# Kernel tuning notes

Hardware: AMD Instinct MI355X
Metric: run time of the kernel (lower is better)

## Reference

```python
import jax, jax.numpy as jnp
import numpy as np

# ---- config (matches init_kwargs) ----
B, NP, DIM, HEADS, DH, NDIM = 32, 576, 512, 8, 64, 16
N = NP + 1                 # seq len incl cls token = 577
INNER = HEADS * DH         # 512


def setup_inputs() -> dict:
    key = jax.random.key(0)
    ks = jax.random.split(key, 11)
    D2 = 2 * DIM  # bidirectional EMA doubles kernel dim
    return {
        "x": jax.random.normal(ks[0], (B, N, DIM), jnp.float32),
        "W_qk": jax.random.normal(ks[1], (DIM, 2 * INNER), jnp.float32) / np.float32(np.sqrt(DIM)),
        "W_v": jax.random.normal(ks[2], (DIM, INNER), jnp.float32) / np.float32(np.sqrt(DIM)),
        "W_out": jax.random.normal(ks[3], (INNER, DIM), jnp.float32) / np.float32(np.sqrt(INNER)),
        "b_out": jnp.zeros((DIM,), jnp.float32),
        "rel_bias": jax.random.normal(ks[4], (2 * N - 1,), jnp.float32) * 0.02,
        "ema_delta": jax.random.normal(ks[5], (D2, NDIM, 1), jnp.float32),
        "ema_alpha": jax.random.normal(ks[6], (D2, NDIM, 1), jnp.float32),
        "ema_beta": jax.random.normal(ks[7], (D2, NDIM, 1), jnp.float32) * 0.5,
        "ema_gamma": jax.random.normal(ks[8], (D2, NDIM), jnp.float32) * 0.5,
        "ema_omega": jax.random.normal(ks[9], (DIM,), jnp.float32),
    }


def _ema_move(x, delta, alpha, beta, gamma, omega):
    """Bidirectional MultiHeadEMA (MEGA) via FFT convolution. x: (B, L, D)."""
    b, L, d = x.shape
    scale = jnp.asarray(np.sqrt(1.0 / NDIM), x.dtype)
    p = jax.nn.sigmoid(delta)                      # (2D, N, 1)
    q = 1.0 - p * jax.nn.sigmoid(alpha)            # (2D, N, 1), in (0,1)
    vander = jnp.arange(L, dtype=x.dtype)[None, None, :] * jnp.log(q)  # (2D, N, L)
    kern = (p * beta) * jnp.exp(vander)            # (2D, N, L)
    k = jnp.einsum('dnl,dn->dl', kern, gamma * scale)  # (2D, L)
    k1, k2 = k[:d], k[d:]
    # combined bidirectional kernel, length 2L-1
    kk = jnp.pad(k1, ((0, 0), (L - 1, 0))) + jnp.pad(k2[:, ::-1], ((0, 0), (0, L - 1)))
    xt = jnp.pad(x.transpose(0, 2, 1), ((0, 0), (0, 0), (L - 1, 0)))  # (B, D, 2L-1)
    fft_len = 2 * L - 1
    nfft = 2 * fft_len
    out = jnp.fft.irfft(jnp.fft.rfft(xt, n=nfft) * jnp.fft.rfft(kk, n=nfft)[None], n=nfft)
    s = 2 * L - 2
    out = out[..., s:s + L].transpose(0, 2, 1).astype(x.dtype)  # (B, L, D)
    return jax.nn.silu(out + x * omega)


def _rel_pos_bias(rb, seq_len):
    """RelativePositionalBias (MEGA): (2*N-1,) param -> (seq_len, seq_len) bias."""
    max_pos = N
    bvec = rb[max_pos - seq_len: max_pos + seq_len - 1]   # (2*seq_len-1,)
    t = jnp.pad(bvec, (0, seq_len))
    t = jnp.tile(t, seq_len)[:-seq_len].reshape(seq_len, 3 * seq_len - 2)
    r = (2 * seq_len - 1) // 2
    return t[:, r:t.shape[1] - r]


def reference(x, W_qk, W_v, W_out, b_out, rel_bias,
              ema_delta, ema_alpha, ema_beta, ema_gamma, ema_omega):
    b, n, _ = x.shape
    cls_tok = x[:, :1]
    moved = _ema_move(x[:, 1:], ema_delta, ema_alpha, ema_beta, ema_gamma, ema_omega)
    xm = jnp.concatenate([cls_tok, moved], axis=1)        # (B, N, DIM)
    q, k = jnp.split(xm @ W_qk, 2, axis=-1)
    v = xm @ W_v                                          # smooth_v_as_well=True

    def heads(t):
        return t.reshape(b, n, HEADS, DH).transpose(0, 2, 1, 3)  # (B, H, N, DH)

    q, k, v = heads(q), heads(k), heads(v)
    dots = jnp.einsum('bhid,bhjd->bhij', q, k) * (DH ** -0.5)
    attn = jax.nn.softmax(dots, axis=-1)
    attn = attn + _rel_pos_bias(rel_bias, n)[None, None]  # bias added AFTER softmax
    out = jnp.einsum('bhij,bhjd->bhid', attn, v)
    out = out.transpose(0, 2, 1, 3).reshape(b, n, INNER)
    return out @ W_out + b_out
```

## Files before the change

### kernel.cpp

```cpp
#include <hip/hip_runtime.h>

typedef unsigned short ushort;

typedef __bf16 bf16x8 __attribute__((ext_vector_type(8)));
typedef float  f32x4  __attribute__((ext_vector_type(4)));
typedef unsigned short u16x8 __attribute__((ext_vector_type(8)));
typedef unsigned short u16x4 __attribute__((ext_vector_type(4)));

static constexpr int BB   = 32;
static constexpr int NN   = 577;
static constexpr int LL   = 576;
static constexpr int DIMC = 512;
static constexpr int BN   = BB * NN;

static constexpr size_t SZ_WQKVT = 1536ull * 512 * 2;
static constexpr size_t SZ_WOUTT = 512ull * 512 * 2;
static constexpr size_t SZ_QK    = (size_t)BN * 1024 * 2;
static constexpr size_t SZ_V     = (size_t)BN * 512 * 2;
static constexpr size_t SZ_VT    = 256ull * 64 * 640 * 2;
static constexpr size_t OFF_WQKVT = 0;
static constexpr size_t OFF_WOUTT = OFF_WQKVT + SZ_WQKVT;
static constexpr size_t OFF_QTAB  = OFF_WOUTT + SZ_WOUTT;
static constexpr size_t OFF_CTAB  = OFF_QTAB + 65536;
static constexpr size_t OFF_QK    = OFF_CTAB + 65536;
static constexpr size_t OFF_V     = OFF_QK + SZ_QK;
static constexpr size_t OFF_REGION= OFF_V + SZ_V;
static constexpr size_t OFF_XM    = OFF_REGION;
static constexpr size_t OFF_VT    = OFF_REGION;
static constexpr size_t OFF_AO    = OFF_REGION + SZ_VT;
static constexpr size_t WS_NEEDED = OFF_AO + SZ_V;

__device__ __forceinline__ ushort bf16bits(float f) {
  unsigned int u = __builtin_bit_cast(unsigned int, f);
  u = (u + 0x7fffu + ((u >> 16) & 1u)) >> 16;
  return (ushort)u;
}
__device__ __forceinline__ float sigmoidf_(float z) { return 1.f / (1.f + __expf(-z)); }
__device__ __forceinline__ float siluf(float z)     { return z / (1.f + __expf(-z)); }
__device__ __forceinline__ float redsum16(float v) {
  v += __shfl_xor(v, 1); v += __shfl_xor(v, 2);
  v += __shfl_xor(v, 4); v += __shfl_xor(v, 8);
  return v;
}

__global__ __launch_bounds__(256) void k_prep(
    const float* __restrict__ delta, const float* __restrict__ alpha,
    const float* __restrict__ beta,  const float* __restrict__ gamma,
    const float* __restrict__ Wqk,   const float* __restrict__ Wv,
    const float* __restrict__ Wout,
    float* __restrict__ qtab, float* __restrict__ ctab,
    ushort* __restrict__ Wqkvt, ushort* __restrict__ Woutt)
{
  int idx = blockIdx.x * 256 + threadIdx.x;
  if (idx < 16384) {
    float p = sigmoidf_(delta[idx]);
    float q = 1.f - p * sigmoidf_(alpha[idx]);
    qtab[idx] = q;
    ctab[idx] = p * beta[idx] * gamma[idx] * 0.25f;
  }
  int i2 = idx - 16384;
  if (i2 >= 0 && i2 < 1536 * 512) {
    int n = i2 >> 9, k = i2 & 511;
    float w = (n < 1024) ? Wqk[k * 1024 + n] : Wv[k * 512 + (n - 1024)];
    Wqkvt[i2] = bf16bits(w);
  }
  int i3 = i2 - 1536 * 512;
  if (i3 >= 0 && i3 < 512 * 512) {
    int n = i3 >> 9, k = i3 & 511;
    Woutt[i3] = bf16bits(Wout[k * 512 + n]);
  }
}

__global__ __launch_bounds__(64) void k_ema_scan(
    const float* __restrict__ x, const float* __restrict__ qtab,
    const float* __restrict__ ctab, float* __restrict__ y1, float* __restrict__ y2)
{
  const int bx = blockIdx.x;
  const int b  = blockIdx.y;
  if (bx < 8) {
    const int d = bx * 64 + threadIdx.x;
    float q[16], c[16], h[16];
    #pragma unroll
    for (int n = 0; n < 16; ++n) { q[n] = qtab[d*16+n]; c[n] = ctab[d*16+n]; h[n] = 0.f; }
    const float* xp = x  + ((size_t)b * NN + 1) * DIMC + d;
    float*       yp = y1 + ((size_t)b * LL)     * DIMC + d;
    float xn[8];
    #pragma unroll
    for (int u = 0; u < 8; ++u) xn[u] = xp[u * DIMC];
    for (int blk = 0; blk < 72; ++blk) {
      float xv[8];
      #pragma unroll
      for (int u = 0; u < 8; ++u) xv[u] = xn[u];
      if (blk < 71) {
        #pragma unroll
        for (int u = 0; u < 8; ++u) xn[u] = xp[((blk + 1) * 8 + u) * DIMC];
      }
      #pragma unroll
      for (int u = 0; u < 8; ++u) {
        float xx = xv[u], y = 0.f;
        #pragma unroll
        for (int n = 0; n < 16; ++n) { h[n] = fmaf(q[n], h[n], xx); y = fmaf(c[n], h[n], y); }
        yp[(blk * 8 + u) * DIMC] = y;
      }
    }
  } else {
    const int d = (bx - 8) * 64 + threadIdx.x;
    float q[16], c[16], g[16];
    #pragma unroll
    for (int n = 0; n < 16; ++n) { q[n] = qtab[(d+512)*16+n]; c[n] = ctab[(d+512)*16+n]; g[n] = 0.f; }
    const float* xp = x  + ((size_t)b * NN + 1) * DIMC + d;
    float*       yp = y2 + ((size_t)b * LL)     * DIMC + d;
    float xn[8];
    #pragma unroll
    for (int u = 0; u < 8; ++u) xn[u] = xp[(568 + u) * DIMC];
    for (int blk = 71; blk >= 0; --blk) {
      float xv[8];
      #pragma unroll
      for (int u = 0; u < 8; ++u) xv[u] = xn[u];
      if (blk > 0) {
        #pragma unroll
        for (int u = 0; u < 8; ++u) xn[u] = xp[((blk - 1) * 8 + u) * DIMC];
      }
      #pragma unroll
      for (int u = 7; u >= 0; --u) {
        float xx = xv[u], y = 0.f;
        #pragma unroll
        for (int n = 0; n < 16; ++n) { g[n] = fmaf(q[n], g[n], xx); y = fmaf(c[n], g[n], y); }
        yp[(blk * 8 + u) * DIMC] = y;
      }
    }
  }
}

__global__ __launch_bounds__(256) void k_ema_comb(
    const float* __restrict__ x, const float* __restrict__ y1,
    const float* __restrict__ y2, const float* __restrict__ omega,
    ushort* __restrict__ xm)
{
  size_t v = (size_t)blockIdx.x * 256 + threadIdx.x;
  size_t e = v * 4;
  int n = (int)(e >> 9);
  int d = (int)(e & 511);
  int b = n / 577;
  int i = n - b * 577;
  f32x4 xv = *(const f32x4*)(x + e);
  u16x4 o;
  if (i == 0) {
    #pragma unroll
    for (int k = 0; k < 4; ++k) o[k] = bf16bits(xv[k]);
  } else {
    size_t ey = ((size_t)b * LL + (i - 1)) * DIMC + d;
    f32x4 a  = *(const f32x4*)(y1 + ey);
    f32x4 c2 = *(const f32x4*)(y2 + ey);
    f32x4 om = *(const f32x4*)(omega + d);
    #pragma unroll
    for (int k = 0; k < 4; ++k) o[k] = bf16bits(siluf(a[k] + c2[k] + xv[k] * om[k]));
  }
  *(u16x4*)(xm + e) = o;
}

__global__ __launch_bounds__(256) void k_qkv(
    const ushort* __restrict__ A, const ushort* __restrict__ Bt,
    ushort* __restrict__ qk, ushort* __restrict__ v)
{
  __shared__ alignas(16) ushort lA[128 * 40];
  __shared__ alignas(16) ushort lB[128 * 40];
  const int tid = threadIdx.x, wv = tid >> 6, lane = tid & 63;
  const int quad = lane >> 4, c16 = lane & 15;
  const int row0 = blockIdx.y * 128, n0 = blockIdx.x * 128;
  const int wm = (wv >> 1) * 64, wn = (wv & 1) * 64;
  f32x4 z4 = {0.f, 0.f, 0.f, 0.f};
  f32x4 acc[4][4];
  #pragma unroll
  for (int mi = 0; mi < 4; ++mi)
    #pragma unroll
    for (int ni = 0; ni < 4; ++ni) acc[mi][ni] = z4;

  for (int kt = 0; kt < 16; ++kt) {
    const int k0 = kt * 32;
    u16x8 sa[2], sb[2];
    #pragma unroll
    for (int it = 0; it < 2; ++it) {
      int ch = it * 256 + tid;
      int r = ch >> 2, cc = ch & 3;
      int grow = row0 + r; if (grow > BN - 1) grow = BN - 1;
      sa[it] = *(const u16x8*)(A + (size_t)grow * 512 + k0 + cc * 8);
      sb[it] = *(const u16x8*)(Bt + (size_t)(n0 + r) * 512 + k0 + cc * 8);
    }
    __syncthreads();
    #pragma unroll
    for (int it = 0; it < 2; ++it) {
      int ch = it * 256 + tid;
      int r = ch >> 2, cc = ch & 3;
      *(u16x8*)(lA + r * 40 + cc * 8) = sa[it];
      *(u16x8*)(lB + r * 40 + cc * 8) = sb[it];
    }
    __syncthreads();
    bf16x8 af[4], bfv[4];
    #pragma unroll
    for (int mi = 0; mi < 4; ++mi)
      af[mi] = *(const bf16x8*)(lA + (wm + mi * 16 + c16) * 40 + quad * 8);
    #pragma unroll
    for (int ni = 0; ni < 4; ++ni)
      bfv[ni] = *(const bf16x8*)(lB + (wn + ni * 16 + c16) * 40 + quad * 8);
    #pragma unroll
    for (int mi = 0; mi < 4; ++mi)
      #pragma unroll
      for (int ni = 0; ni < 4; ++ni)
        acc[mi][ni] = __builtin_amdgcn_mfma_f32_16x16x32_bf16(af[mi], bfv[ni], acc[mi][ni], 0, 0, 0);
  }
  const bool isv = (n0 >= 1024);
  const float osc = (n0 < 512) ? 0.125f : 1.0f;
  #pragma unroll
  for (int mi = 0; mi < 4; ++mi) {
    #pragma unroll
    for (int r = 0; r < 4; ++r) {
      int grow = row0 + wm + mi * 16 + quad * 4 + r;
      if (grow < BN) {
        #pragma unroll
        for (int ni = 0; ni < 4; ++ni) {
          int col = n0 + wn + ni * 16 + c16;
          ushort vb = bf16bits(acc[mi][ni][r] * osc);
          if (!isv) qk[(size_t)grow * 1024 + col] = vb;
          else      v[(size_t)grow * 512 + (col - 1024)] = vb;
        }
      }
    }
  }
}

__global__ __launch_bounds__(256) void k_vtrans(
    const ushort* __restrict__ v, ushort* __restrict__ vt)
{
  __shared__ alignas(16) ushort lt[64 * 72];
  const int tid = threadIdx.x;
  const int bh = blockIdx.y, b = bh >> 3, h = bh & 7;
  const int j0 = blockIdx.x * 64;
  #pragma unroll
  for (int pass = 0; pass < 2; ++pass) {
    int cch = pass * 256 + tid;
    int jl = cch >> 3, cc = cch & 7;
    int gj = j0 + jl;
    u16x8 val = {0, 0, 0, 0, 0, 0, 0, 0};
    if (gj < 577) val = *(const u16x8*)(v + ((size_t)(b * NN + gj)) * 512 + h * 64 + cc * 8);
    *(u16x8*)(lt + jl * 72 + cc * 8) = val;
  }
  __syncthreads();
  #pragma unroll
  for (int pass = 0; pass < 2; ++pass) {
    int cch = pass * 256 + tid;
    int dh = cch >> 3, jc = cch & 7;
    u16x8 o;
    #pragma unroll
    for (int e = 0; e < 8; ++e) o[e] = lt[(jc * 8 + e) * 72 + dh];
    *(u16x8*)(vt + ((size_t)(bh * 64 + dh)) * 640 + j0 + jc * 8) = o;
  }
}

__global__ __launch_bounds__(256) void k_fattn(
    const ushort* __restrict__ qk, const ushort* __restrict__ vt,
    const float* __restrict__ relb, ushort* __restrict__ ao)
{
  __shared__ alignas(16) ushort lq[128 * 64];
  __shared__ alignas(16) ushort lk[64 * 64];
  __shared__ alignas(16) ushort lv[64 * 64];
  __shared__ alignas(16) ushort lp[128 * 64];
  __shared__ ushort lbias16[1280];
  const int tid = threadIdx.x, wv = tid >> 6, lane = tid & 63;
  const int quad = lane >> 4, c16 = lane & 15;
  const int hc16 = c16 >> 3, lo16 = c16 & 7;
  const int bh = blockIdx.y, b = bh >> 3, h = bh & 7;
  const int i0 = blockIdx.x * 128, wm = wv * 32;
  for (int t = tid; t < 1280; t += 256) {
    int idx = t - 64;
    lbias16[t] = (idx >= 0 && idx < 1153) ? bf16bits(relb[idx]) : (ushort)0;
  }
  #pragma unroll
  for (int it = 0; it < 4; ++it) {
    int ch = it * 256 + tid;
    int r = ch >> 3, cc = ch & 7;
    int gi = i0 + r; if (gi > 576) gi = 576;
    *(u16x8*)(lq + r * 64 + ((cc ^ (r & 7)) * 8)) =
        *(const u16x8*)(qk + ((size_t)(b * NN + gi)) * 1024 + h * 64 + cc * 8);
  }
  float lsum[2][4];
  #pragma unroll
  for (int ms = 0; ms < 2; ++ms)
    #pragma unroll
    for (int r = 0; r < 4; ++r) lsum[ms][r] = 0.f;
  f32x4 z4 = {0.f, 0.f, 0.f, 0.f};
  f32x4 accp[2][4], accb[2][4];
  #pragma unroll
  for (int ms = 0; ms < 2; ++ms)
    #pragma unroll
    for (int ns = 0; ns < 4; ++ns) { accp[ms][ns] = z4; accb[ms][ns] = z4; }

  for (int jt = 0; jt < 10; ++jt) {
    const int j0 = jt * 64;
    u16x8 sk[2], sv[2];
    #pragma unroll
    for (int it = 0; it < 2; ++it) {
      int ch = it * 256 + tid;
      int r = ch >> 3, cc = ch & 7;
      int gj = j0 + r; if (gj > 576) gj = 576;
      sk[it] = *(const u16x8*)(qk + ((size_t)(b * NN + gj)) * 1024 + 512 + h * 64 + cc * 8);
      sv[it] = *(const u16x8*)(vt + ((size_t)(bh * 64 + r)) * 640 + j0 + cc * 8);
    }
    __syncthreads();
    #pragma unroll
    for (int it = 0; it < 2; ++it) {
      int ch = it * 256 + tid;
      int r = ch >> 3, cc = ch & 7;
      int pc = (cc ^ (r & 7)) * 8;
      *(u16x8*)(lk + r * 64 + pc) = sk[it];
      *(u16x8*)(lv + r * 64 + pc) = sv[it];
    }
    __syncthreads();
    f32x4 dacc[2][4];
    #pragma unroll
    for (int ms = 0; ms < 2; ++ms)
      #pragma unroll
      for (int ns = 0; ns < 4; ++ns) dacc[ms][ns] = z4;
    #pragma unroll
    for (int kk = 0; kk < 2; ++kk) {
      bf16x8 aq[2], bk[4];
      const int ck = kk * 4 + quad;
      #pragma unroll
      for (int ms = 0; ms < 2; ++ms) {
        const int row = wm + ms * 16 + c16;
        aq[ms] = *(const bf16x8*)(lq + row * 64 + ((ck ^ (row & 7)) * 8));
      }
      #pragma unroll
      for (int ns = 0; ns < 4; ++ns) {
        const int row = ns * 16 + c16;
        bk[ns] = *(const bf16x8*)(lk + row * 64 + ((ck ^ (row & 7)) * 8));
      }
      #pragma unroll
      for (int ms = 0; ms < 2; ++ms)
        #pragma unroll
        for (int ns = 0; ns < 4; ++ns)
          dacc[ms][ns] = __builtin_amdgcn_mfma_f32_16x16x32_bf16(aq[ms], bk[ns], dacc[ms][ns], 0, 0, 0);
    }
    #pragma unroll
    for (int ms = 0; ms < 2; ++ms) {
      #pragma unroll
      for (int r = 0; r < 4; ++r) {
        float ex[4];
        #pragma unroll
        for (int ns = 0; ns < 4; ++ns) {
          float e = __expf(dacc[ms][ns][r]);
          if (jt == 9 && (j0 + ns * 16 + c16) >= 577) e = 0.f;
          ex[ns] = e;
        }
        lsum[ms][r] += (ex[0] + ex[1]) + (ex[2] + ex[3]);
        const int lrow = wm + ms * 16 + quad * 4 + r;
        const int xr = lrow & 7;
        #pragma unroll
        for (int ns = 0; ns < 4; ++ns)
          lp[lrow * 64 + (((ns * 2 + hc16) ^ xr) * 8) + lo16] = bf16bits(ex[ns]);
      }
    }
    __syncthreads();
    #pragma unroll
    for (int kk = 0; kk < 2; ++kk) {
      bf16x8 ap[2], ab[2], bV[4];
      const int ck = kk * 4 + quad;
      #pragma unroll
      for (int ms = 0; ms < 2; ++ms) {
        const int row = wm + ms * 16 + c16;
        ap[ms] = *(const bf16x8*)(lp + row * 64 + ((ck ^ (row & 7)) * 8));
      }
      #pragma unroll
      for (int ms = 0; ms < 2; ++ms) {
        u16x8 abu;
        const int base = 64 + 576 + j0 + kk * 32 + quad * 8 - (i0 + wm + ms * 16 + c16);
        #pragma unroll
        for (int e = 0; e < 8; ++e) abu[e] = lbias16[base + e];
        ab[ms] = __builtin_bit_cast(bf16x8, abu);
      }
      #pragma unroll
      for (int ns = 0; ns < 4; ++ns) {
        const int row = ns * 16 + c16;
        bV[ns] = *(const bf16x8*)(lv + row * 64 + ((ck ^ (row & 7)) * 8));
      }
      #pragma unroll
      for (int ms = 0; ms < 2; ++ms)
        #pragma unroll
        for (int ns = 0; ns < 4; ++ns) {
          accp[ms][ns] = __builtin_amdgcn_mfma_f32_16x16x32_bf16(ap[ms], bV[ns], accp[ms][ns], 0, 0, 0);
          accb[ms][ns] = __builtin_amdgcn_mfma_f32_16x16x32_bf16(ab[ms], bV[ns], accb[ms][ns], 0, 0, 0);
        }
    }
  }
  float li[2][4];
  #pragma unroll
  for (int ms = 0; ms < 2; ++ms)
    #pragma unroll
    for (int r = 0; r < 4; ++r) li[ms][r] = 1.f / redsum16(lsum[ms][r]);
  #pragma unroll
  for (int ms = 0; ms < 2; ++ms)
    #pragma unroll
    for (int r = 0; r < 4; ++r) {
      int ii = i0 + wm + ms * 16 + quad * 4 + r;
      if (ii < 577) {
        #pragma unroll
        for (int ns = 0; ns < 4; ++ns)
          ao[((size_t)(b * NN + ii)) * 512 + h * 64 + ns * 16 + c16] =
              bf16bits(accp[ms][ns][r] * li[ms][r] + accb[ms][ns][r]);
      }
    }
}

__global__ __launch_bounds__(256) void k_out(
    const ushort* __restrict__ A, const ushort* __restrict__ Bt,
    const float* __restrict__ bout, float* __restrict__ out)
{
  __shared__ alignas(16) ushort lA[128 * 40];
  __shared__ alignas(16) ushort lB[128 * 40];
  const int tid = threadIdx.x, wv = tid >> 6, lane = tid & 63;
  const int quad = lane >> 4, c16 = lane & 15;
  const int row0 = blockIdx.y * 128, n0 = blockIdx.x * 128;
  const int wm = (wv >> 1) * 64, wn = (wv & 1) * 64;
  f32x4 z4 = {0.f, 0.f, 0.f, 0.f};
  f32x4 acc[4][4];
  #pragma unroll
  for (int mi = 0; mi < 4; ++mi)
    #pragma unroll
    for (int ni = 0; ni < 4; ++ni) acc[mi][ni] = z4;

  for (int kt = 0; kt < 16; ++kt) {
    const int k0 = kt * 32;
    u16x8 sa[2], sb[2];
    #pragma unroll
    for (int it = 0; it < 2; ++it) {
      int ch = it * 256 + tid;
      int r = ch >> 2, cc = ch & 3;
      int grow = row0 + r; if (grow > BN - 1) grow = BN - 1;
      sa[it] = *(const u16x8*)(A + (size_t)grow * 512 + k0 + cc * 8);
      sb[it] = *(const u16x8*)(Bt + (size_t)(n0 + r) * 512 + k0 + cc * 8);
    }
    __syncthreads();
    #pragma unroll
    for (int it = 0; it < 2; ++it) {
      int ch = it * 256 + tid;
      int r = ch >> 2, cc = ch & 3;
      *(u16x8*)(lA + r * 40 + cc * 8) = sa[it];
      *(u16x8*)(lB + r * 40 + cc * 8) = sb[it];
    }
    __syncthreads();
    bf16x8 af[4], bfv[4];
    #pragma unroll
    for (int mi = 0; mi < 4; ++mi)
      af[mi] = *(const bf16x8*)(lA + (wm + mi * 16 + c16) * 40 + quad * 8);
    #pragma unroll
    for (int ni = 0; ni < 4; ++ni)
      bfv[ni] = *(const bf16x8*)(lB + (wn + ni * 16 + c16) * 40 + quad * 8);
    #pragma unroll
    for (int mi = 0; mi < 4; ++mi)
      #pragma unroll
      for (int ni = 0; ni < 4; ++ni)
        acc[mi][ni] = __builtin_amdgcn_mfma_f32_16x16x32_bf16(af[mi], bfv[ni], acc[mi][ni], 0, 0, 0);
  }
  #pragma unroll
  for (int mi = 0; mi < 4; ++mi) {
    #pragma unroll
    for (int r = 0; r < 4; ++r) {
      int grow = row0 + wm + mi * 16 + quad * 4 + r;
      if (grow < BN) {
        #pragma unroll
        for (int ni = 0; ni < 4; ++ni) {
          int col = n0 + wn + ni * 16 + c16;
          out[(size_t)grow * 512 + col] = acc[mi][ni][r] + bout[col];
        }
      }
    }
  }
}

extern "C" void kernel_launch(void* const* d_in, const int* in_sizes, int n_in,
                              void* d_out, int out_size, void* d_ws, size_t ws_size,
                              hipStream_t stream) {
  (void)in_sizes; (void)n_in; (void)out_size;
  if (ws_size < WS_NEEDED) return;
  const float* x    = (const float*)d_in[0];
  const float* Wqk  = (const float*)d_in[1];
  const float* Wv   = (const float*)d_in[2];
  const float* Wout = (const float*)d_in[3];
  const float* bout = (const float*)d_in[4];
  const float* relb = (const float*)d_in[5];
  const float* edel = (const float*)d_in[6];
  const float* ealp = (const float*)d_in[7];
  const float* ebet = (const float*)d_in[8];
  const float* egam = (const float*)d_in[9];
  const float* eome = (const float*)d_in[10];

  char* ws = (char*)d_ws;
  ushort* Wqkvt = (ushort*)(ws + OFF_WQKVT);
  ushort* Woutt = (ushort*)(ws + OFF_WOUTT);
  float*  qtab  = (float*)(ws + OFF_QTAB);
  float*  ctab  = (float*)(ws + OFF_CTAB);
  ushort* qkb   = (ushort*)(ws + OFF_QK);
  ushort* vb    = (ushort*)(ws + OFF_V);
  ushort* xm    = (ushort*)(ws + OFF_XM);
  ushort* vtb   = (ushort*)(ws + OFF_VT);
  ushort* aob   = (ushort*)(ws + OFF_AO);
  float*  outp  = (float*)d_out;
  float*  y1    = outp;
  float*  y2    = (float*)(ws + OFF_QK);

  k_prep<<<dim3(4160), dim3(256), 0, stream>>>(edel, ealp, ebet, egam, Wqk, Wv, Wout,
                                               qtab, ctab, Wqkvt, Woutt);
  k_ema_scan<<<dim3(16, 32), dim3(64), 0, stream>>>(x, qtab, ctab, y1, y2);
  k_ema_comb<<<dim3(9232), dim3(256), 0, stream>>>(x, y1, y2, eome, xm);
  k_qkv<<<dim3(12, 145), dim3(256), 0, stream>>>(xm, Wqkvt, qkb, vb);
  k_vtrans<<<dim3(10, 256), dim3(256), 0, stream>>>(vb, vtb);
  k_fattn<<<dim3(5, 256), dim3(256), 0, stream>>>(qkb, vtb, relb, aob);
  k_out<<<dim3(4, 145), dim3(256), 0, stream>>>(aob, Woutt, bout, outp);
}
```

Baseline: 364.8 us.

## Prefetch next K-tiles in GEMMs and split rel-bias@V into separate kernel

```diff
diff --git a/kernel.cpp b/kernel.cpp
--- a/kernel.cpp
+++ b/kernel.cpp
@@ -35,6 +35,10 @@
   u = (u + 0x7fffu + ((u >> 16) & 1u)) >> 16;
   return (ushort)u;
 }
+__device__ __forceinline__ float bf2f(ushort u) {
+  unsigned int x = ((unsigned int)u) << 16;
+  return __builtin_bit_cast(float, x);
+}
 __device__ __forceinline__ float sigmoidf_(float z) { return 1.f / (1.f + __expf(-z)); }
 __device__ __forceinline__ float siluf(float z)     { return z / (1.f + __expf(-z)); }
 __device__ __forceinline__ float redsum16(float v) {
@@ -176,17 +180,16 @@
     #pragma unroll
     for (int ni = 0; ni < 4; ++ni) acc[mi][ni] = z4;
 
+  u16x8 sa[2], sb[2];
+  #pragma unroll
+  for (int it = 0; it < 2; ++it) {
+    int ch = it * 256 + tid;
+    int r = ch >> 2, cc = ch & 3;
+    int grow = row0 + r; if (grow > BN - 1) grow = BN - 1;
+    sa[it] = *(const u16x8*)(A + (size_t)grow * 512 + cc * 8);
+    sb[it] = *(const u16x8*)(Bt + (size_t)(n0 + r) * 512 + cc * 8);
+  }
   for (int kt = 0; kt < 16; ++kt) {
-    const int k0 = kt * 32;
-    u16x8 sa[2], sb[2];
-    #pragma unroll
-    for (int it = 0; it < 2; ++it) {
-      int ch = it * 256 + tid;
-      int r = ch >> 2, cc = ch & 3;
-      int grow = row0 + r; if (grow > BN - 1) grow = BN - 1;
-      sa[it] = *(const u16x8*)(A + (size_t)grow * 512 + k0 + cc * 8);
-      sb[it] = *(const u16x8*)(Bt + (size_t)(n0 + r) * 512 + k0 + cc * 8);
-    }
     __syncthreads();
     #pragma unroll
     for (int it = 0; it < 2; ++it) {
@@ -196,6 +199,17 @@
       *(u16x8*)(lB + r * 40 + cc * 8) = sb[it];
     }
     __syncthreads();
+    if (kt < 15) {
+      const int k0 = (kt + 1) * 32;
+      #pragma unroll
+      for (int it = 0; it < 2; ++it) {
+        int ch = it * 256 + tid;
+        int r = ch >> 2, cc = ch & 3;
+        int grow = row0 + r; if (grow > BN - 1) grow = BN - 1;
+        sa[it] = *(const u16x8*)(A + (size_t)grow * 512 + k0 + cc * 8);
+        sb[it] = *(const u16x8*)(Bt + (size_t)(n0 + r) * 512 + k0 + cc * 8);
+      }
+    }
     bf16x8 af[4], bfv[4];
     #pragma unroll
     for (int mi = 0; mi < 4; ++mi)
@@ -257,55 +271,134 @@
   }
 }
 
-__global__ __launch_bounds__(256) void k_fattn(
+__global__ __launch_bounds__(256, 4) void k_biasv(
+    const ushort* __restrict__ vt, const float* __restrict__ relb,
+    ushort* __restrict__ ao)
+{
+  __shared__ alignas(16) ushort lv[64 * 64];
+  __shared__ ushort lbias16[1280];
+  const int tid = threadIdx.x, wv = tid >> 6, lane = tid & 63;
+  const int quad = lane >> 4, c16 = lane & 15;
+  const int bh = blockIdx.y, b = bh >> 3, h = bh & 7;
+  const int i0 = blockIdx.x * 128, wm = wv * 32;
+  for (int t = tid; t < 1280; t += 256) {
+    int idx = t - 64;
+    lbias16[t] = (idx >= 0 && idx < 1153) ? bf16bits(relb[idx]) : (ushort)0;
+  }
+  f32x4 z4 = {0.f, 0.f, 0.f, 0.f};
+  f32x4 acc[2][4];
+  #pragma unroll
+  for (int ms = 0; ms < 2; ++ms)
+    #pragma unroll
+    for (int ns = 0; ns < 4; ++ns) acc[ms][ns] = z4;
+
+  u16x8 sv[2];
+  #pragma unroll
+  for (int it = 0; it < 2; ++it) {
+    int ch = it * 256 + tid;
+    int r = ch >> 3, cc = ch & 7;
+    sv[it] = *(const u16x8*)(vt + ((size_t)(bh * 64 + r)) * 640 + cc * 8);
+  }
+  for (int jt = 0; jt < 10; ++jt) {
+    const int j0 = jt * 64;
+    __syncthreads();
+    #pragma unroll
+    for (int it = 0; it < 2; ++it) {
+      int ch = it * 256 + tid;
+      int r = ch >> 3, cc = ch & 7;
+      *(u16x8*)(lv + r * 64 + ((cc ^ (r & 7)) * 8)) = sv[it];
+    }
+    __syncthreads();
+    if (jt < 9) {
+      #pragma unroll
+      for (int it = 0; it < 2; ++it) {
+        int ch = it * 256 + tid;
+        int r = ch >> 3, cc = ch & 7;
+        sv[it] = *(const u16x8*)(vt + ((size_t)(bh * 64 + r)) * 640 + j0 + 64 + cc * 8);
+      }
+    }
+    #pragma unroll
+    for (int kk = 0; kk < 2; ++kk) {
+      bf16x8 ab[2], bV[4];
+      const int ck = kk * 4 + quad;
+      #pragma unroll
+      for (int ms = 0; ms < 2; ++ms) {
+        u16x8 abu;
+        const int base = 64 + 576 + j0 + kk * 32 + quad * 8 - (i0 + wm + ms * 16 + c16);
+        #pragma unroll
+        for (int e = 0; e < 8; ++e) abu[e] = lbias16[base + e];
+        ab[ms] = __builtin_bit_cast(bf16x8, abu);
+      }
+      #pragma unroll
+      for (int ns = 0; ns < 4; ++ns) {
+        const int row = ns * 16 + c16;
+        bV[ns] = *(const bf16x8*)(lv + row * 64 + ((ck ^ (row & 7)) * 8));
+      }
+      #pragma unroll
+      for (int ms = 0; ms < 2; ++ms)
+        #pragma unroll
+        for (int ns = 0; ns < 4; ++ns)
+          acc[ms][ns] = __builtin_amdgcn_mfma_f32_16x16x32_bf16(ab[ms], bV[ns], acc[ms][ns], 0, 0, 0);
+    }
+  }
+  #pragma unroll
+  for (int ms = 0; ms < 2; ++ms)
+    #pragma unroll
+    for (int r = 0; r < 4; ++r) {
+      int ii = i0 + wm + ms * 16 + quad * 4 + r;
+      if (ii < 577) {
+        #pragma unroll
+        for (int ns = 0; ns < 4; ++ns)
+          ao[((size_t)(b * NN + ii)) * 512 + h * 64 + ns * 16 + c16] =
+              bf16bits(acc[ms][ns][r]);
+      }
+    }
+}
+
+__global__ __launch_bounds__(256, 4) void k_fattn(
     const ushort* __restrict__ qk, const ushort* __restrict__ vt,
-    const float* __restrict__ relb, ushort* __restrict__ ao)
-{
-  __shared__ alignas(16) ushort lq[128 * 64];
+    ushort* __restrict__ ao)
+{
   __shared__ alignas(16) ushort lk[64 * 64];
   __shared__ alignas(16) ushort lv[64 * 64];
   __shared__ alignas(16) ushort lp[128 * 64];
-  __shared__ ushort lbias16[1280];
   const int tid = threadIdx.x, wv = tid >> 6, lane = tid & 63;
   const int quad = lane >> 4, c16 = lane & 15;
   const int hc16 = c16 >> 3, lo16 = c16 & 7;
   const int bh = blockIdx.y, b = bh >> 3, h = bh & 7;
   const int i0 = blockIdx.x * 128, wm = wv * 32;
-  for (int t = tid; t < 1280; t += 256) {
-    int idx = t - 64;
-    lbias16[t] = (idx >= 0 && idx < 1153) ? bf16bits(relb[idx]) : (ushort)0;
-  }
-  #pragma unroll
-  for (int it = 0; it < 4; ++it) {
+  bf16x8 aq[2][2];
+  #pragma unroll
+  for (int ms = 0; ms < 2; ++ms) {
+    int gi = i0 + wm + ms * 16 + c16; if (gi > 576) gi = 576;
+    const ushort* qrow = qk + ((size_t)(b * NN + gi)) * 1024 + h * 64;
+    #pragma unroll
+    for (int kk = 0; kk < 2; ++kk)
+      aq[ms][kk] = *(const bf16x8*)(qrow + kk * 32 + quad * 8);
+  }
+  float lsum[2][4];
+  #pragma unroll
+  for (int ms = 0; ms < 2; ++ms)
+    #pragma unroll
+    for (int r = 0; r < 4; ++r) lsum[ms][r] = 0.f;
+  f32x4 z4 = {0.f, 0.f, 0.f, 0.f};
+  f32x4 accp[2][4];
+  #pragma unroll
+  for (int ms = 0; ms < 2; ++ms)
+    #pragma unroll
+    for (int ns = 0; ns < 4; ++ns) accp[ms][ns] = z4;
+
+  u16x8 sk[2], sv[2];
+  #pragma unroll
+  for (int it = 0; it < 2; ++it) {
     int ch = it * 256 + tid;
     int r = ch >> 3, cc = ch & 7;
-    int gi = i0 + r; if (gi > 576) gi = 576;
-    *(u16x8*)(lq + r * 64 + ((cc ^ (r & 7)) * 8)) =
-        *(const u16x8*)(qk + ((size_t)(b * NN + gi)) * 1024 + h * 64 + cc * 8);
-  }
-  float lsum[2][4];
-  #pragma unroll
-  for (int ms = 0; ms < 2; ++ms)
-    #pragma unroll
-    for (int r = 0; r < 4; ++r) lsum[ms][r] = 0.f;
-  f32x4 z4 = {0.f, 0.f, 0.f, 0.f};
-  f32x4 accp[2][4], accb[2][4];
-  #pragma unroll
-  for (int ms = 0; ms < 2; ++ms)
-    #pragma unroll
-    for (int ns = 0; ns < 4; ++ns) { accp[ms][ns] = z4; accb[ms][ns] = z4; }
-
+    int gj = r; if (gj > 576) gj = 576;
+    sk[it] = *(const u16x8*)(qk + ((size_t)(b * NN + gj)) * 1024 + 512 + h * 64 + cc * 8);
+    sv[it] = *(const u16x8*)(vt + ((size_t)(bh * 64 + r)) * 640 + cc * 8);
+  }
   for (int jt = 0; jt < 10; ++jt) {
     const int j0 = jt * 64;
-    u16x8 sk[2], sv[2];
-    #pragma unroll
-    for (int it = 0; it < 2; ++it) {
-      int ch = it * 256 + tid;
-      int r = ch >> 3, cc = ch & 7;
-      int gj = j0 + r; if (gj > 576) gj = 576;
-      sk[it] = *(const u16x8*)(qk + ((size_t)(b * NN + gj)) * 1024 + 512 + h * 64 + cc * 8);
-      sv[it] = *(const u16x8*)(vt + ((size_t)(bh * 64 + r)) * 640 + j0 + cc * 8);
-    }
     __syncthreads();
     #pragma unroll
     for (int it = 0; it < 2; ++it) {
@@ -316,6 +409,17 @@
       *(u16x8*)(lv + r * 64 + pc) = sv[it];
     }
     __syncthreads();
+    if (jt < 9) {
+      const int jn = j0 + 64;
+      #pragma unroll
+      for (int it = 0; it < 2; ++it) {
+        int ch = it * 256 + tid;
+        int r = ch >> 3, cc = ch & 7;
+        int gj = jn + r; if (gj > 576) gj = 576;
+        sk[it] = *(const u16x8*)(qk + ((size_t)(b * NN + gj)) * 1024 + 512 + h * 64 + cc * 8);
+        sv[it] = *(const u16x8*)(vt + ((size_t)(bh * 64 + r)) * 640 + jn + cc * 8);
+      }
+    }
     f32x4 dacc[2][4];
     #pragma unroll
     for (int ms = 0; ms < 2; ++ms)
@@ -323,13 +427,8 @@
       for (int ns = 0; ns < 4; ++ns) dacc[ms][ns] = z4;
     #pragma unroll
     for (int kk = 0; kk < 2; ++kk) {
-      bf16x8 aq[2], bk[4];
+      bf16x8 bk[4];
       const int ck = kk * 4 + quad;
-      #pragma unroll
-      for (int ms = 0; ms < 2; ++ms) {
-        const int row = wm + ms * 16 + c16;
-        aq[ms] = *(const bf16x8*)(lq + row * 64 + ((ck ^ (row & 7)) * 8));
-      }
       #pragma unroll
       for (int ns = 0; ns < 4; ++ns) {
         const int row = ns * 16 + c16;
@@ -339,7 +438,7 @@
       for (int ms = 0; ms < 2; ++ms)
         #pragma unroll
         for (int ns = 0; ns < 4; ++ns)
-          dacc[ms][ns] = __builtin_amdgcn_mfma_f32_16x16x32_bf16(aq[ms], bk[ns], dacc[ms][ns], 0, 0, 0);
+          dacc[ms][ns] = __builtin_amdgcn_mfma_f32_16x16x32_bf16(aq[ms][kk], bk[ns], dacc[ms][ns], 0, 0, 0);
     }
     #pragma unroll
     for (int ms = 0; ms < 2; ++ms) {
@@ -363,7 +462,7 @@
     __syncthreads();
     #pragma unroll
     for (int kk = 0; kk < 2; ++kk) {
-      bf16x8 ap[2], ab[2], bV[4];
+      bf16x8 ap[2], bV[4];
       const int ck = kk * 4 + quad;
       #pragma unroll
       for (int ms = 0; ms < 2; ++ms) {
@@ -371,14 +470,6 @@
         ap[ms] = *(const bf16x8*)(lp + row * 64 + ((ck ^ (row & 7)) * 8));
       }
       #pragma unroll
-      for (int ms = 0; ms < 2; ++ms) {
-        u16x8 abu;
-        const int base = 64 + 576 + j0 + kk * 32 + quad * 8 - (i0 + wm + ms * 16 + c16);
-        #pragma unroll
-        for (int e = 0; e < 8; ++e) abu[e] = lbias16[base + e];
-        ab[ms] = __builtin_bit_cast(bf16x8, abu);
-      }
-      #pragma unroll
       for (int ns = 0; ns < 4; ++ns) {
         const int row = ns * 16 + c16;
         bV[ns] = *(const bf16x8*)(lv + row * 64 + ((ck ^ (row & 7)) * 8));
@@ -386,10 +477,8 @@
       #pragma unroll
       for (int ms = 0; ms < 2; ++ms)
         #pragma unroll
-        for (int ns = 0; ns < 4; ++ns) {
+        for (int ns = 0; ns < 4; ++ns)
           accp[ms][ns] = __builtin_amdgcn_mfma_f32_16x16x32_bf16(ap[ms], bV[ns], accp[ms][ns], 0, 0, 0);
-          accb[ms][ns] = __builtin_amdgcn_mfma_f32_16x16x32_bf16(ab[ms], bV[ns], accb[ms][ns], 0, 0, 0);
-        }
     }
   }
   float li[2][4];
@@ -404,9 +493,11 @@
       int ii = i0 + wm + ms * 16 + quad * 4 + r;
       if (ii < 577) {
         #pragma unroll
-        for (int ns = 0; ns < 4; ++ns)
-          ao[((size_t)(b * NN + ii)) * 512 + h * 64 + ns * 16 + c16] =
-              bf16bits(accp[ms][ns][r] * li[ms][r] + accb[ms][ns][r]);
+        for (int ns = 0; ns < 4; ++ns) {
+          size_t idx = ((size_t)(b * NN + ii)) * 512 + h * 64 + ns * 16 + c16;
+          float ob = bf2f(ao[idx]);
+          ao[idx] = bf16bits(fmaf(accp[ms][ns][r], li[ms][r], ob));
+        }
       }
     }
 }
@@ -428,17 +519,16 @@
     #pragma unroll
     for (int ni = 0; ni < 4; ++ni) acc[mi][ni] = z4;
 
+  u16x8 sa[2], sb[2];
+  #pragma unroll
+  for (int it = 0; it < 2; ++it) {
+    int ch = it * 256 + tid;
+    int r = ch >> 2, cc = ch & 3;
+    int grow = row0 + r; if (grow > BN - 1) grow = BN - 1;
+    sa[it] = *(const u16x8*)(A + (size_t)grow * 512 + cc * 8);
+    sb[it] = *(const u16x8*)(Bt + (size_t)(n0 + r) * 512 + cc * 8);
+  }
   for (int kt = 0; kt < 16; ++kt) {
-    const int k0 = kt * 32;
-    u16x8 sa[2], sb[2];
-    #pragma unroll
-    for (int it = 0; it < 2; ++it) {
-      int ch = it * 256 + tid;
-      int r = ch >> 2, cc = ch & 3;
-      int grow = row0 + r; if (grow > BN - 1) grow = BN - 1;
-      sa[it] = *(const u16x8*)(A + (size_t)grow * 512 + k0 + cc * 8);
-      sb[it] = *(const u16x8*)(Bt + (size_t)(n0 + r) * 512 + k0 + cc * 8);
-    }
     __syncthreads();
     #pragma unroll
     for (int it = 0; it < 2; ++it) {
@@ -448,6 +538,17 @@
       *(u16x8*)(lB + r * 40 + cc * 8) = sb[it];
     }
     __syncthreads();
+    if (kt < 15) {
+      const int k0 = (kt + 1) * 32;
+      #pragma unroll
+      for (int it = 0; it < 2; ++it) {
+        int ch = it * 256 + tid;
+        int r = ch >> 2, cc = ch & 3;
+        int grow = row0 + r; if (grow > BN - 1) grow = BN - 1;
+        sa[it] = *(const u16x8*)(A + (size_t)grow * 512 + k0 + cc * 8);
+        sb[it] = *(const u16x8*)(Bt + (size_t)(n0 + r) * 512 + k0 + cc * 8);
+      }
+    }
     bf16x8 af[4], bfv[4];
     #pragma unroll
     for (int mi = 0; mi < 4; ++mi)
@@ -514,6 +615,7 @@
   k_ema_comb<<<dim3(9232), dim3(256), 0, stream>>>(x, y1, y2, eome, xm);
   k_qkv<<<dim3(12, 145), dim3(256), 0, stream>>>(xm, Wqkvt, qkb, vb);
   k_vtrans<<<dim3(10, 256), dim3(256), 0, stream>>>(vb, vtb);
-  k_fattn<<<dim3(5, 256), dim3(256), 0, stream>>>(qkb, vtb, relb, aob);
+  k_biasv<<<dim3(5, 256), dim3(256), 0, stream>>>(vtb, relb, aob);
+  k_fattn<<<dim3(5, 256), dim3(256), 0, stream>>>(qkb, vtb, aob);
   k_out<<<dim3(4, 145), dim3(256), 0, stream>>>(aob, Woutt, bout, outp);
 }
```

Result: slower. 548.0 us (+50.2%).

## Prefetch next tile into registers in GEMM and attention kernels; keep Q in registers

Applied to the files above, without the earlier changes.

```diff
diff --git a/kernel.cpp b/kernel.cpp
--- a/kernel.cpp
+++ b/kernel.cpp
@@ -176,17 +176,16 @@
     #pragma unroll
     for (int ni = 0; ni < 4; ++ni) acc[mi][ni] = z4;
 
+  u16x8 sa[2], sb[2];
+  #pragma unroll
+  for (int it = 0; it < 2; ++it) {
+    int ch = it * 256 + tid;
+    int r = ch >> 2, cc = ch & 3;
+    int grow = row0 + r; if (grow > BN - 1) grow = BN - 1;
+    sa[it] = *(const u16x8*)(A + (size_t)grow * 512 + cc * 8);
+    sb[it] = *(const u16x8*)(Bt + (size_t)(n0 + r) * 512 + cc * 8);
+  }
   for (int kt = 0; kt < 16; ++kt) {
-    const int k0 = kt * 32;
-    u16x8 sa[2], sb[2];
-    #pragma unroll
-    for (int it = 0; it < 2; ++it) {
-      int ch = it * 256 + tid;
-      int r = ch >> 2, cc = ch & 3;
-      int grow = row0 + r; if (grow > BN - 1) grow = BN - 1;
-      sa[it] = *(const u16x8*)(A + (size_t)grow * 512 + k0 + cc * 8);
-      sb[it] = *(const u16x8*)(Bt + (size_t)(n0 + r) * 512 + k0 + cc * 8);
-    }
     __syncthreads();
     #pragma unroll
     for (int it = 0; it < 2; ++it) {
@@ -196,6 +195,17 @@
       *(u16x8*)(lB + r * 40 + cc * 8) = sb[it];
     }
     __syncthreads();
+    if (kt < 15) {
+      const int k0 = (kt + 1) * 32;
+      #pragma unroll
+      for (int it = 0; it < 2; ++it) {
+        int ch = it * 256 + tid;
+        int r = ch >> 2, cc = ch & 3;
+        int grow = row0 + r; if (grow > BN - 1) grow = BN - 1;
+        sa[it] = *(const u16x8*)(A + (size_t)grow * 512 + k0 + cc * 8);
+        sb[it] = *(const u16x8*)(Bt + (size_t)(n0 + r) * 512 + k0 + cc * 8);
+      }
+    }
     bf16x8 af[4], bfv[4];
     #pragma unroll
     for (int mi = 0; mi < 4; ++mi)
@@ -261,7 +271,6 @@
     const ushort* __restrict__ qk, const ushort* __restrict__ vt,
     const float* __restrict__ relb, ushort* __restrict__ ao)
 {
-  __shared__ alignas(16) ushort lq[128 * 64];
   __shared__ alignas(16) ushort lk[64 * 64];
   __shared__ alignas(16) ushort lv[64 * 64];
   __shared__ alignas(16) ushort lp[128 * 64];
@@ -275,13 +284,14 @@
     int idx = t - 64;
     lbias16[t] = (idx >= 0 && idx < 1153) ? bf16bits(relb[idx]) : (ushort)0;
   }
-  #pragma unroll
-  for (int it = 0; it < 4; ++it) {
-    int ch = it * 256 + tid;
-    int r = ch >> 3, cc = ch & 7;
-    int gi = i0 + r; if (gi > 576) gi = 576;
-    *(u16x8*)(lq + r * 64 + ((cc ^ (r & 7)) * 8)) =
-        *(const u16x8*)(qk + ((size_t)(b * NN + gi)) * 1024 + h * 64 + cc * 8);
+  bf16x8 aq[2][2];
+  #pragma unroll
+  for (int ms = 0; ms < 2; ++ms) {
+    int gi = i0 + wm + ms * 16 + c16; if (gi > 576) gi = 576;
+    const ushort* qrow = qk + ((size_t)(b * NN + gi)) * 1024 + h * 64;
+    #pragma unroll
+    for (int kk = 0; kk < 2; ++kk)
+      aq[ms][kk] = *(const bf16x8*)(qrow + kk * 32 + quad * 8);
   }
   float lsum[2][4];
   #pragma unroll
@@ -295,17 +305,17 @@
     #pragma unroll
     for (int ns = 0; ns < 4; ++ns) { accp[ms][ns] = z4; accb[ms][ns] = z4; }
 
+  u16x8 sk[2], sv[2];
+  #pragma unroll
+  for (int it = 0; it < 2; ++it) {
+    int ch = it * 256 + tid;
+    int r = ch >> 3, cc = ch & 7;
+    int gj = r; if (gj > 576) gj = 576;
+    sk[it] = *(const u16x8*)(qk + ((size_t)(b * NN + gj)) * 1024 + 512 + h * 64 + cc * 8);
+    sv[it] = *(const u16x8*)(vt + ((size_t)(bh * 64 + r)) * 640 + cc * 8);
+  }
   for (int jt = 0; jt < 10; ++jt) {
     const int j0 = jt * 64;
-    u16x8 sk[2], sv[2];
-    #pragma unroll
-    for (int it = 0; it < 2; ++it) {
-      int ch = it * 256 + tid;
-      int r = ch >> 3, cc = ch & 7;
-      int gj = j0 + r; if (gj > 576) gj = 576;
-      sk[it] = *(const u16x8*)(qk + ((size_t)(b * NN + gj)) * 1024 + 512 + h * 64 + cc * 8);
-      sv[it] = *(const u16x8*)(vt + ((size_t)(bh * 64 + r)) * 640 + j0 + cc * 8);
-    }
     __syncthreads();
     #pragma unroll
     for (int it = 0; it < 2; ++it) {
@@ -316,6 +326,17 @@
       *(u16x8*)(lv + r * 64 + pc) = sv[it];
     }
     __syncthreads();
+    if (jt < 9) {
+      const int jn = j0 + 64;
+      #pragma unroll
+      for (int it = 0; it < 2; ++it) {
+        int ch = it * 256 + tid;
+        int r = ch >> 3, cc = ch & 7;
+        int gj = jn + r; if (gj > 576) gj = 576;
+        sk[it] = *(const u16x8*)(qk + ((size_t)(b * NN + gj)) * 1024 + 512 + h * 64 + cc * 8);
+        sv[it] = *(const u16x8*)(vt + ((size_t)(bh * 64 + r)) * 640 + jn + cc * 8);
+      }
+    }
     f32x4 dacc[2][4];
     #pragma unroll
     for (int ms = 0; ms < 2; ++ms)
@@ -323,13 +344,8 @@
       for (int ns = 0; ns < 4; ++ns) dacc[ms][ns] = z4;
     #pragma unroll
     for (int kk = 0; kk < 2; ++kk) {
-      bf16x8 aq[2], bk[4];
+      bf16x8 bk[4];
       const int ck = kk * 4 + quad;
-      #pragma unroll
-      for (int ms = 0; ms < 2; ++ms) {
-        const int row = wm + ms * 16 + c16;
-        aq[ms] = *(const bf16x8*)(lq + row * 64 + ((ck ^ (row & 7)) * 8));
-      }
       #pragma unroll
       for (int ns = 0; ns < 4; ++ns) {
         const int row = ns * 16 + c16;
@@ -339,7 +355,7 @@
       for (int ms = 0; ms < 2; ++ms)
         #pragma unroll
         for (int ns = 0; ns < 4; ++ns)
-          dacc[ms][ns] = __builtin_amdgcn_mfma_f32_16x16x32_bf16(aq[ms], bk[ns], dacc[ms][ns], 0, 0, 0);
+          dacc[ms][ns] = __builtin_amdgcn_mfma_f32_16x16x32_bf16(aq[ms][kk], bk[ns], dacc[ms][ns], 0, 0, 0);
     }
     #pragma unroll
     for (int ms = 0; ms < 2; ++ms) {
@@ -406,7 +422,7 @@
         #pragma unroll
         for (int ns = 0; ns < 4; ++ns)
           ao[((size_t)(b * NN + ii)) * 512 + h * 64 + ns * 16 + c16] =
-              bf16bits(accp[ms][ns][r] * li[ms][r] + accb[ms][ns][r]);
+              bf16bits(fmaf(accp[ms][ns][r], li[ms][r], accb[ms][ns][r]));
       }
     }
 }
@@ -428,17 +444,16 @@
     #pragma unroll
     for (int ni = 0; ni < 4; ++ni) acc[mi][ni] = z4;
 
+  u16x8 sa[2], sb[2];
+  #pragma unroll
+  for (int it = 0; it < 2; ++it) {
+    int ch = it * 256 + tid;
+    int r = ch >> 2, cc = ch & 3;
+    int grow = row0 + r; if (grow > BN - 1) grow = BN - 1;
+    sa[it] = *(const u16x8*)(A + (size_t)grow * 512 + cc * 8);
+    sb[it] = *(const u16x8*)(Bt + (size_t)(n0 + r) * 512 + cc * 8);
+  }
   for (int kt = 0; kt < 16; ++kt) {
-    const int k0 = kt * 32;
-    u16x8 sa[2], sb[2];
-    #pragma unroll
-    for (int it = 0; it < 2; ++it) {
-      int ch = it * 256 + tid;
-      int r = ch >> 2, cc = ch & 3;
-      int grow = row0 + r; if (grow > BN - 1) grow = BN - 1;
-      sa[it] = *(const u16x8*)(A + (size_t)grow * 512 + k0 + cc * 8);
-      sb[it] = *(const u16x8*)(Bt + (size_t)(n0 + r) * 512 + k0 + cc * 8);
-    }
     __syncthreads();
     #pragma unroll
     for (int it = 0; it < 2; ++it) {
@@ -448,6 +463,17 @@
       *(u16x8*)(lB + r * 40 + cc * 8) = sb[it];
     }
     __syncthreads();
+    if (kt < 15) {
+      const int k0 = (kt + 1) * 32;
+      #pragma unroll
+      for (int it = 0; it < 2; ++it) {
+        int ch = it * 256 + tid;
+        int r = ch >> 2, cc = ch & 3;
+        int grow = row0 + r; if (grow > BN - 1) grow = BN - 1;
+        sa[it] = *(const u16x8*)(A + (size_t)grow * 512 + k0 + cc * 8);
+        sb[it] = *(const u16x8*)(Bt + (size_t)(n0 + r) * 512 + k0 + cc * 8);
+      }
+    }
     bf16x8 af[4], bfv[4];
     #pragma unroll
     for (int mi = 0; mi < 4; ++mi)
```

Measured after the change: 367.5 us. About the same (+0.7%).
